# Optimization experiments

Measured on AMD Instinct MI355X. Metric: run time of the kernel, lower is better.

## Reference

```python
import jax, jax.numpy as jnp
import numpy as np

B, CIN, H, W = 32, 64, 112, 112
COUT, KH, KW = 64, 3, 3
STRIDE = (1, 1)
PADDING = ((1, 1), (1, 1))
DILATION = (1, 1)


def setup_inputs() -> dict:
    key = jax.random.key(0)
    k1, k2, k3 = jax.random.split(key, 3)
    # quantized activations and weights, int8 value range [-128, 127]
    x_q = jax.random.randint(k1, (B, CIN, H, W), -128, 128, dtype=jnp.int32).astype(jnp.int8)
    w_q = jax.random.randint(k2, (COUT, CIN, KH, KW), -128, 128, dtype=jnp.int32).astype(jnp.int8)
    weight_scale = jnp.float32(0.02)   # per-tensor weight scale
    act_scale = jnp.float32(0.05)      # per-tensor activation scale
    bias = jax.random.normal(k3, (COUT,), dtype=jnp.float32)
    return {"x_q": x_q, "w_q": w_q, "weight_scale": weight_scale,
            "act_scale": act_scale, "bias": bias}


def reference(x_q, w_q, weight_scale, act_scale, bias):
    acc = jax.lax.conv_general_dilated(
        x_q.astype(jnp.int32), w_q.astype(jnp.int32),
        window_strides=STRIDE, padding=PADDING, rhs_dilation=DILATION,
        dimension_numbers=("NCHW", "OIHW", "NCHW"),
        preferred_element_type=jnp.int32)
    # fused dequant (per-tensor scales) + FP32 bias -> FP32 output [B, COUT, H, W]
    out = acc.astype(jnp.float32) * (act_scale * weight_scale) + bias[None, :, None, None]
    return out
```

## Files before the change

kernel.cpp:

```cpp
#include <hip/hip_runtime.h>
#include <stdint.h>

#define BATCH 32
#define CIN   64
#define HH    112
#define WW    112
#define COUT_ 64

typedef int v4i __attribute__((ext_vector_type(4)));

#define WT_OFF   0

__global__ void wtrans_kernel(const int* __restrict__ wq, int8_t* __restrict__ wt) {
    int idx = blockIdx.x * 256 + threadIdx.x;
    int ci   = idx & 63;
    int khkw = (idx >> 6) % 9;
    int co   = idx / 576;
    wt[idx] = (int8_t)wq[co * 576 + ci * 9 + khkw];
}

__launch_bounds__(256, 2)
__global__ void conv4_kernel(const int* __restrict__ x,
                             const int8_t* __restrict__ wt,
                             const float*  __restrict__ wscale,
                             const float*  __restrict__ ascale,
                             const float*  __restrict__ bias,
                             float*        __restrict__ out) {
    __shared__ int8_t xs[8 * 114 * 64];

    const int tid = threadIdx.x;
    const int b   = blockIdx.x >> 3;
    const int hb  = (blockIdx.x & 7) * 14;

    const int lane = tid & 63;
    const int wave = tid >> 6;
    const int ln15 = lane & 15;
    const int quad = lane >> 4;

    {
        int pr   = tid >> 5;
        int side = (tid >> 4) & 1;
        int d    = tid & 15;
        *(uint32_t*)&xs[pr * 7296 + (side ? 113 : 0) * 64 + d * 4] = 0u;
    }

    const v4i* wrow = (const v4i*)(wt + (size_t)(wave * 16 + ln15) * 576);
    v4i a[9];
    #pragma unroll
    for (int t = 0; t < 9; ++t) a[t] = wrow[t * 4 + quad];

    const float s = ascale[0] * wscale[0];
    float bv[4];
    #pragma unroll
    for (int reg = 0; reg < 4; ++reg) bv[reg] = bias[wave * 16 + quad * 4 + reg];

    v4i q[16];
    auto stage_load = [&](int hstart) {
        #pragma unroll
        for (int it = 0; it < 4; ++it) {
            #pragma unroll
            for (int p = 0; p < 4; ++p) q[it * 4 + p] = (v4i){0, 0, 0, 0};
            int job = tid + it * 256;
            if (job < 896) {
                int ci4  = job & 15;
                int cg   = (job >> 4) % 28;
                int row2 = job / 448;
                int hh   = hstart + row2;
                if (hh >= 0 && hh < HH) {
                    const v4i* gp = (const v4i*)
                        (x + ((size_t)(b * CIN + ci4 * 4) * HH + hh) * WW + cg * 4);
                    q[it * 4 + 0] = gp[0];
                    q[it * 4 + 1] = gp[3136];
                    q[it * 4 + 2] = gp[2 * 3136];
                    q[it * 4 + 3] = gp[3 * 3136];
                }
            }
        }
    };
    auto stage_write = [&](int pb) {
        #pragma unroll
        for (int it = 0; it < 4; ++it) {
            int job = tid + it * 256;
            if (job < 896) {
                int ci4  = job & 15;
                int cg   = (job >> 4) % 28;
                int row2 = job / 448;
                int pr   = (pb + row2) & 7;
                int8_t* rowp = &xs[pr * 7296];
                #pragma unroll
                for (int j = 0; j < 4; ++j) {
                    uint32_t lo01 = __builtin_amdgcn_perm(
                        (uint32_t)q[it * 4 + 1][j], (uint32_t)q[it * 4 + 0][j], 0x0C0C0400u);
                    uint32_t lo23 = __builtin_amdgcn_perm(
                        (uint32_t)q[it * 4 + 3][j], (uint32_t)q[it * 4 + 2][j], 0x04000C0Cu);
                    int col = cg * 4 + 1 + j;
                    int sd  = (((ci4 >> 2) ^ ((col >> 1) & 3)) << 2) | (ci4 & 3);
                    *(uint32_t*)&rowp[col * 64 + sd * 4] = lo01 | lo23;
                }
            }
        }
    };

    stage_load(hb - 1);
    asm volatile("s_waitcnt vmcnt(0)" ::: "memory");
    stage_write(0);
    stage_load(hb + 1);
    asm volatile("s_waitcnt vmcnt(0)" ::: "memory");
    stage_write(2);
    asm volatile("s_waitcnt lgkmcnt(0)" ::: "memory");
    __builtin_amdgcn_s_barrier();
    __builtin_amdgcn_sched_barrier(0);

    #pragma unroll 1
    for (int t = 0; t < 7; ++t) {
        if (t < 6) {
            stage_load(hb + 2 * t + 3);
            __builtin_amdgcn_sched_barrier(0);
        }

        v4i acc[2][7];
        #pragma unroll
        for (int r = 0; r < 2; ++r)
            #pragma unroll
            for (int nt = 0; nt < 7; ++nt)
                acc[r][nt] = (v4i){0, 0, 0, 0};

        #pragma unroll
        for (int rho = 0; rho < 4; ++rho) {
            const int pr = (2 * t + rho) & 7;
            #pragma unroll
            for (int kw = 0; kw < 3; ++kw) {
                const int m   = ln15 + kw;
                const int swz = (quad ^ ((m >> 1) & 3)) << 4;
                const int8_t* bp = &xs[pr * 7296 + m * 64 + swz];
                #pragma unroll
                for (int nt = 0; nt < 7; ++nt) {
                    v4i bfrag = *(const v4i*)(bp + nt * 1024);
                    if (rho <= 2)
                        acc[0][nt] = __builtin_amdgcn_mfma_i32_16x16x64_i8(
                            a[rho * 3 + kw], bfrag, acc[0][nt], 0, 0, 0);
                    if (rho >= 1)
                        acc[1][nt] = __builtin_amdgcn_mfma_i32_16x16x64_i8(
                            a[(rho - 1) * 3 + kw], bfrag, acc[1][nt], 0, 0, 0);
                }
            }
        }

        __builtin_amdgcn_sched_barrier(0);
        if (t < 6) {
            asm volatile("s_waitcnt vmcnt(0)" ::: "memory");
            stage_write((2 * t + 4) & 7);
            asm volatile("s_waitcnt lgkmcnt(0)" ::: "memory");
            __builtin_amdgcn_s_barrier();
            __builtin_amdgcn_sched_barrier(0);
        }

        const int h0 = hb + 2 * t;
        #pragma unroll
        for (int r = 0; r < 2; ++r) {
            const int h = h0 + r;
            #pragma unroll
            for (int reg = 0; reg < 4; ++reg) {
                int co = wave * 16 + quad * 4 + reg;
                float* op = out + ((size_t)(b * COUT_ + co) * HH + h) * WW;
                #pragma unroll
                for (int nt = 0; nt < 7; ++nt)
                    op[nt * 16 + ln15] = (float)acc[r][nt][reg] * s + bv[reg];
            }
        }
    }
}

extern "C" void kernel_launch(void* const* d_in, const int* in_sizes, int n_in,
                              void* d_out, int out_size, void* d_ws, size_t ws_size,
                              hipStream_t stream) {
    const int*    xq     = (const int*)d_in[0];
    const int*    wq     = (const int*)d_in[1];
    const float*  wscale = (const float*)d_in[2];
    const float*  ascale = (const float*)d_in[3];
    const float*  bias   = (const float*)d_in[4];
    int8_t* wt  = (int8_t*)d_ws;
    float*  out = (float*)d_out;

    wtrans_kernel<<<144, 256, 0, stream>>>(wq, wt);
    conv4_kernel<<<256, 256, 0, stream>>>(xq, wt, wscale, ascale, bias, out);
}
```

Before: 200.3 us.

## Split conv into 4-row tiles across 896 blocks with smaller LDS ring

Each block now computes 4 output rows instead of 14, raising the grid from 256 to 896 blocks so the GPU's compute units are better filled. The LDS buffer shrinks from 8 to 6 padded rows, which allows more resident blocks per CU. The block index is remapped so consecutive blocks spread across batches and row groups. In exchange, each block loads a larger share of halo rows relative to its output (6 input rows for 4 output rows), and the pipelined loop becomes a fixed two-step sequence with less overlap.

New measurement: 208.3 us. 1.04x slower.

```diff
diff --git a/kernel.cpp b/kernel.cpp
--- a/kernel.cpp
+++ b/kernel.cpp
@@ -9,7 +9,6 @@
 
 typedef int v4i __attribute__((ext_vector_type(4)));
 
-#define WT_OFF   0
 
 __global__ void wtrans_kernel(const int* __restrict__ wq, int8_t* __restrict__ wt) {
     int idx = blockIdx.x * 256 + threadIdx.x;
@@ -20,24 +19,25 @@
 }
 
 __launch_bounds__(256, 2)
-__global__ void conv4_kernel(const int* __restrict__ x,
+__global__ void conv5_kernel(const int* __restrict__ x,
                              const int8_t* __restrict__ wt,
                              const float*  __restrict__ wscale,
                              const float*  __restrict__ ascale,
                              const float*  __restrict__ bias,
                              float*        __restrict__ out) {
-    __shared__ int8_t xs[8 * 114 * 64];
+    __shared__ int8_t xs[6 * 114 * 64];
 
     const int tid = threadIdx.x;
-    const int b   = blockIdx.x >> 3;
-    const int hb  = (blockIdx.x & 7) * 14;
+    const int bt = ((blockIdx.x & 7) * 112) + (blockIdx.x >> 3);
+    const int b  = bt / 28;
+    const int hb = (bt % 28) * 4;
 
     const int lane = tid & 63;
     const int wave = tid >> 6;
     const int ln15 = lane & 15;
     const int quad = lane >> 4;
 
-    {
+    if (tid < 192) {
         int pr   = tid >> 5;
         int side = (tid >> 4) & 1;
         int d    = tid & 15;
@@ -85,8 +85,7 @@
                 int ci4  = job & 15;
                 int cg   = (job >> 4) % 28;
                 int row2 = job / 448;
-                int pr   = (pb + row2) & 7;
-                int8_t* rowp = &xs[pr * 7296];
+                int8_t* rowp = &xs[(pb + row2) * 7296];
                 #pragma unroll
                 for (int j = 0; j < 4; ++j) {
                     uint32_t lo01 = __builtin_amdgcn_perm(
@@ -101,33 +100,16 @@
         }
     };
 
-    stage_load(hb - 1);
-    asm volatile("s_waitcnt vmcnt(0)" ::: "memory");
-    stage_write(0);
-    stage_load(hb + 1);
-    asm volatile("s_waitcnt vmcnt(0)" ::: "memory");
-    stage_write(2);
-    asm volatile("s_waitcnt lgkmcnt(0)" ::: "memory");
-    __builtin_amdgcn_s_barrier();
-    __builtin_amdgcn_sched_barrier(0);
-
-    #pragma unroll 1
-    for (int t = 0; t < 7; ++t) {
-        if (t < 6) {
-            stage_load(hb + 2 * t + 3);
-            __builtin_amdgcn_sched_barrier(0);
-        }
-
-        v4i acc[2][7];
+    v4i acc[2][7];
+    auto mfma_tile = [&](int rbase) {
         #pragma unroll
         for (int r = 0; r < 2; ++r)
             #pragma unroll
             for (int nt = 0; nt < 7; ++nt)
                 acc[r][nt] = (v4i){0, 0, 0, 0};
-
         #pragma unroll
         for (int rho = 0; rho < 4; ++rho) {
-            const int pr = (2 * t + rho) & 7;
+            const int pr = rbase + rho;
             #pragma unroll
             for (int kw = 0; kw < 3; ++kw) {
                 const int m   = ln15 + kw;
@@ -145,17 +127,8 @@
                 }
             }
         }
-
-        __builtin_amdgcn_sched_barrier(0);
-        if (t < 6) {
-            asm volatile("s_waitcnt vmcnt(0)" ::: "memory");
-            stage_write((2 * t + 4) & 7);
-            asm volatile("s_waitcnt lgkmcnt(0)" ::: "memory");
-            __builtin_amdgcn_s_barrier();
-            __builtin_amdgcn_sched_barrier(0);
-        }
-
-        const int h0 = hb + 2 * t;
+    };
+    auto store_tile = [&](int h0) {
         #pragma unroll
         for (int r = 0; r < 2; ++r) {
             const int h = h0 + r;
@@ -168,7 +141,31 @@
                     op[nt * 16 + ln15] = (float)acc[r][nt][reg] * s + bv[reg];
             }
         }
-    }
+    };
+
+    stage_load(hb - 1);
+    asm volatile("s_waitcnt vmcnt(0)" ::: "memory");
+    stage_write(0);
+    stage_load(hb + 1);
+    asm volatile("s_waitcnt vmcnt(0)" ::: "memory");
+    stage_write(2);
+    asm volatile("s_waitcnt lgkmcnt(0)" ::: "memory");
+    __builtin_amdgcn_s_barrier();
+    __builtin_amdgcn_sched_barrier(0);
+
+    stage_load(hb + 3);
+    __builtin_amdgcn_sched_barrier(0);
+    mfma_tile(0);
+    __builtin_amdgcn_sched_barrier(0);
+    asm volatile("s_waitcnt vmcnt(0)" ::: "memory");
+    stage_write(4);
+    asm volatile("s_waitcnt lgkmcnt(0)" ::: "memory");
+    __builtin_amdgcn_s_barrier();
+    __builtin_amdgcn_sched_barrier(0);
+    store_tile(hb);
+
+    mfma_tile(2);
+    store_tile(hb + 2);
 }
 
 extern "C" void kernel_launch(void* const* d_in, const int* in_sizes, int n_in,
@@ -183,5 +180,5 @@
     float*  out = (float*)d_out;
 
     wtrans_kernel<<<144, 256, 0, stream>>>(wq, wt);
-    conv4_kernel<<<256, 256, 0, stream>>>(xq, wt, wscale, ascale, bias, out);
+    conv5_kernel<<<896, 256, 0, stream>>>(xq, wt, wscale, ascale, bias, out);
 }
```

## Split block into ping-pong warpgroups alternating MFMA compute and load/store

Applied to the files above, without the earlier changes.

Doubles the block to 512 threads organised as two 256-thread groups that alternate phases. In each phase one group runs the MFMA tile at raised priority while the other writes staged input to LDS, issues the next global loads and stores the previous tile's output. The goal is to overlap memory traffic and epilogue stores with matrix compute, which the single-group loop serialised. The cost is a more intricate barrier schedule and more register and wave pressure per CU, with a risk of ring-buffer index or synchronisation errors.

New measurement: 195.9 us. 2.2% less time.

```diff
diff --git a/kernel.cpp b/kernel.cpp
--- a/kernel.cpp
+++ b/kernel.cpp
@@ -9,8 +9,6 @@
 
 typedef int v4i __attribute__((ext_vector_type(4)));
 
-#define WT_OFF   0
-
 __global__ void wtrans_kernel(const int* __restrict__ wq, int8_t* __restrict__ wt) {
     int idx = blockIdx.x * 256 + threadIdx.x;
     int ci   = idx & 63;
@@ -19,8 +17,8 @@
     wt[idx] = (int8_t)wq[co * 576 + ci * 9 + khkw];
 }
 
-__launch_bounds__(256, 2)
-__global__ void conv4_kernel(const int* __restrict__ x,
+__launch_bounds__(512, 2)
+__global__ void conv6_kernel(const int* __restrict__ x,
                              const int8_t* __restrict__ wt,
                              const float*  __restrict__ wscale,
                              const float*  __restrict__ ascale,
@@ -28,16 +26,18 @@
                              float*        __restrict__ out) {
     __shared__ int8_t xs[8 * 114 * 64];
 
-    const int tid = threadIdx.x;
-    const int b   = blockIdx.x >> 3;
-    const int hb  = (blockIdx.x & 7) * 14;
+    const int tid  = threadIdx.x;
+    const int g    = tid >> 8;
+    const int stid = tid & 255;
+    const int b    = blockIdx.x >> 3;
+    const int hb   = (blockIdx.x & 7) * 14;
 
     const int lane = tid & 63;
-    const int wave = tid >> 6;
+    const int wave = (tid >> 6) & 3;
     const int ln15 = lane & 15;
     const int quad = lane >> 4;
 
-    {
+    if (tid < 256) {
         int pr   = tid >> 5;
         int side = (tid >> 4) & 1;
         int d    = tid & 15;
@@ -60,7 +60,7 @@
         for (int it = 0; it < 4; ++it) {
             #pragma unroll
             for (int p = 0; p < 4; ++p) q[it * 4 + p] = (v4i){0, 0, 0, 0};
-            int job = tid + it * 256;
+            int job = stid + it * 256;
             if (job < 896) {
                 int ci4  = job & 15;
                 int cg   = (job >> 4) % 28;
@@ -80,13 +80,12 @@
     auto stage_write = [&](int pb) {
         #pragma unroll
         for (int it = 0; it < 4; ++it) {
-            int job = tid + it * 256;
+            int job = stid + it * 256;
             if (job < 896) {
                 int ci4  = job & 15;
                 int cg   = (job >> 4) % 28;
                 int row2 = job / 448;
-                int pr   = (pb + row2) & 7;
-                int8_t* rowp = &xs[pr * 7296];
+                int8_t* rowp = &xs[((pb & 7) + row2) * 7296];
                 #pragma unroll
                 for (int j = 0; j < 4; ++j) {
                     uint32_t lo01 = __builtin_amdgcn_perm(
@@ -101,33 +100,16 @@
         }
     };
 
-    stage_load(hb - 1);
-    asm volatile("s_waitcnt vmcnt(0)" ::: "memory");
-    stage_write(0);
-    stage_load(hb + 1);
-    asm volatile("s_waitcnt vmcnt(0)" ::: "memory");
-    stage_write(2);
-    asm volatile("s_waitcnt lgkmcnt(0)" ::: "memory");
-    __builtin_amdgcn_s_barrier();
-    __builtin_amdgcn_sched_barrier(0);
-
-    #pragma unroll 1
-    for (int t = 0; t < 7; ++t) {
-        if (t < 6) {
-            stage_load(hb + 2 * t + 3);
-            __builtin_amdgcn_sched_barrier(0);
-        }
-
-        v4i acc[2][7];
+    v4i acc[2][7];
+    auto mfma_tile = [&](int rbase) {
         #pragma unroll
         for (int r = 0; r < 2; ++r)
             #pragma unroll
             for (int nt = 0; nt < 7; ++nt)
                 acc[r][nt] = (v4i){0, 0, 0, 0};
-
         #pragma unroll
         for (int rho = 0; rho < 4; ++rho) {
-            const int pr = (2 * t + rho) & 7;
+            const int pr = (rbase + rho) & 7;
             #pragma unroll
             for (int kw = 0; kw < 3; ++kw) {
                 const int m   = ln15 + kw;
@@ -145,16 +127,8 @@
                 }
             }
         }
-
-        __builtin_amdgcn_sched_barrier(0);
-        if (t < 6) {
-            asm volatile("s_waitcnt vmcnt(0)" ::: "memory");
-            stage_write((2 * t + 4) & 7);
-            asm volatile("s_waitcnt lgkmcnt(0)" ::: "memory");
-            __builtin_amdgcn_s_barrier();
-            __builtin_amdgcn_sched_barrier(0);
-        }
-
+    };
+    auto store_tile = [&](int t) {
         const int h0 = hb + 2 * t;
         #pragma unroll
         for (int r = 0; r < 2; ++r) {
@@ -168,7 +142,36 @@
                     op[nt * 16 + ln15] = (float)acc[r][nt][reg] * s + bv[reg];
             }
         }
+    };
+
+    stage_load(hb - 1 + 2 * g);
+    asm volatile("s_waitcnt vmcnt(0)" ::: "memory");
+    stage_write(2 * g);
+    stage_load(hb + 3 + ((g ^ 1) << 1));
+    asm volatile("s_waitcnt lgkmcnt(0)" ::: "memory");
+    __builtin_amdgcn_s_barrier();
+    __builtin_amdgcn_sched_barrier(0);
+
+    #pragma unroll 1
+    for (int ph = 0; ph < 7; ++ph) {
+        if ((ph & 1) == g) {
+            __builtin_amdgcn_s_setprio(1);
+            mfma_tile(2 * ph);
+            __builtin_amdgcn_s_setprio(0);
+        } else {
+            asm volatile("s_waitcnt vmcnt(0)" ::: "memory");
+            if (ph <= 5) stage_write(2 * ph + 4);
+            if (ph <= 3) stage_load(hb + 2 * ph + 7);
+            if (ph >= 1) store_tile(ph - 1);
+        }
+        __builtin_amdgcn_sched_barrier(0);
+        if (ph < 6) {
+            asm volatile("s_waitcnt lgkmcnt(0)" ::: "memory");
+            __builtin_amdgcn_s_barrier();
+            __builtin_amdgcn_sched_barrier(0);
+        }
     }
+    if (g == 0) store_tile(6);
 }
 
 extern "C" void kernel_launch(void* const* d_in, const int* in_sizes, int n_in,
@@ -183,5 +186,5 @@
     float*  out = (float*)d_out;
 
     wtrans_kernel<<<144, 256, 0, stream>>>(wq, wt);
-    conv4_kernel<<<256, 256, 0, stream>>>(xq, wt, wscale, ascale, bias, out);
+    conv6_kernel<<<256, 512, 0, stream>>>(xq, wt, wscale, ascale, bias, out);
 }
```
